# Optimization experiments

Measured on AMD Instinct MI355X. Metric: run time of the kernel, lower is better.

## Reference

```python
import jax, jax.numpy as jnp
import numpy as np

B, N, H = 4, 1024, 32


def setup_inputs() -> dict:
    key = jax.random.key(0)
    ks = jax.random.split(key, 8)
    weights = jax.random.uniform(ks[0], (B, N), dtype=jnp.float32)
    distances = jax.random.uniform(ks[1], (B, N, N), dtype=jnp.float32)
    # nn.Linear-style params (kaiming-uniform-ish scale: U(-1/sqrt(fan_in), 1/sqrt(fan_in)))
    def lin(k, fan_in, fan_out):
        k1, k2 = jax.random.split(k)
        bound = 1.0 / np.sqrt(fan_in)
        W = jax.random.uniform(k1, (fan_in, fan_out), minval=-bound, maxval=bound, dtype=jnp.float32)
        b = jax.random.uniform(k2, (fan_out,), minval=-bound, maxval=bound, dtype=jnp.float32)
        return W, b
    W1, b1 = lin(ks[2], 3, H)
    W2, b2 = lin(ks[3], H, H)
    W3, b3 = lin(ks[4], H, 1)
    return {"weights": weights, "distances": distances,
            "W1": W1, "b1": b1, "W2": W2, "b2": b2, "W3": W3, "b3": b3}


def reference(weights, distances, W1, b1, W2, b2, W3, b3):
    # Avoid materializing the stacked [B,N,N,3] tensor: since the first layer
    # is linear, split W1 rows and broadcast-add the three contributions.
    # h1[b,i,j,:] = w_i * W1[0] + w_j * W1[1] + d_ij * W1[2] + b1
    wi = weights[:, :, None, None] * W1[0]            # [B,N,1,H]
    wj = weights[:, None, :, None] * W1[1]            # [B,1,N,H]
    h = wi + wj + distances[..., None] * W1[2] + b1   # [B,N,N,H]
    h = jax.nn.relu(h)
    h = jax.nn.relu(jnp.einsum('bijh,hk->bijk', h, W2) + b2)
    out = jnp.einsum('bijh,ho->bijo', h, W3) + b3     # [B,N,N,1]
    return jax.nn.softplus(out[..., 0])               # [B,N,N]
```

## Files before the change

kernel.cpp:

```cpp
#include <hip/hip_runtime.h>

#define HCH 32
#define NDIM 1024

using half8 = __attribute__((ext_vector_type(8))) _Float16;
using floatx16 = __attribute__((ext_vector_type(16))) float;

__global__ __launch_bounds__(256, 4)
void lf_kernel(const float* __restrict__ weights,
               const float* __restrict__ distances,
               const float* __restrict__ W1,
               const float* __restrict__ b1,
               const float* __restrict__ W2,
               const float* __restrict__ b2,
               const float* __restrict__ W3,
               const float* __restrict__ b3,
               float* __restrict__ out,
               int rows_total)
{
    const int lane = threadIdx.x & 63;
    const int row_id = blockIdx.x * 4 + (threadIdx.x >> 6);
    if (row_id >= rows_total) return;

    const int b = row_id >> 10;
    const int i = row_id & (NDIM - 1);

    const int col = lane & 31;
    const int half_id = lane >> 5;
    const int kb = half_id * 8;

    const float wi = weights[row_id];

    float base0[8], c0[8], e0[8], base1[8], c1[8], e1[8];
#pragma unroll
    for (int j = 0; j < 8; ++j) {
        const int ch0 = kb + j;
        const int ch1 = 16 + kb + j;
        base0[j] = fmaf(W1[ch0], wi, b1[ch0]);
        c0[j]    = W1[HCH + ch0];
        e0[j]    = W1[2 * HCH + ch0];
        base1[j] = fmaf(W1[ch1], wi, b1[ch1]);
        c1[j]    = W1[HCH + ch1];
        e1[j]    = W1[2 * HCH + ch1];
    }

    half8 a0, a1;
#pragma unroll
    for (int j = 0; j < 8; ++j) {
        a0[j] = (_Float16)W2[(kb + j) * HCH + col];
        a1[j] = (_Float16)W2[(16 + kb + j) * HCH + col];
    }

    floatx16 cinit;
    float w3r[16];
#pragma unroll
    for (int r = 0; r < 16; ++r) {
        const int rc = (r & 3) + 8 * (r >> 2) + 4 * half_id;
        cinit[r] = b2[rc];
        w3r[r]   = W3[rc];
    }
    const float b3v = b3[0];

    const float* __restrict__ drow = distances + (size_t)(b * NDIM + i) * NDIM;
    const float* __restrict__ wrow = weights + b * NDIM;
    float* __restrict__ orow = out + (size_t)(b * NDIM + i) * NDIM;

    float d_cur  = drow[col];
    float wj_cur = wrow[col];

    for (int j0 = 0; j0 < NDIM; j0 += 32) {
        const int jn = (j0 + 32 < NDIM) ? (j0 + 32 + col) : col;
        const float d_nxt  = drow[jn];
        const float wj_nxt = wrow[jn];

        half8 bf0, bf1;
#pragma unroll
        for (int j = 0; j < 8; ++j) {
            const float h0 = fmaxf(fmaf(e0[j], d_cur, fmaf(c0[j], wj_cur, base0[j])), 0.0f);
            const float h1 = fmaxf(fmaf(e1[j], d_cur, fmaf(c1[j], wj_cur, base1[j])), 0.0f);
            bf0[j] = (_Float16)h0;
            bf1[j] = (_Float16)h1;
        }

        floatx16 acc = __builtin_amdgcn_mfma_f32_32x32x16_f16(a0, bf0, cinit, 0, 0, 0);
        acc = __builtin_amdgcn_mfma_f32_32x32x16_f16(a1, bf1, acc, 0, 0, 0);

        float s0 = 0.0f, s1 = 0.0f, s2 = 0.0f, s3 = 0.0f;
#pragma unroll
        for (int r = 0; r < 16; r += 4) {
            s0 = fmaf(fmaxf(acc[r + 0], 0.0f), w3r[r + 0], s0);
            s1 = fmaf(fmaxf(acc[r + 1], 0.0f), w3r[r + 1], s1);
            s2 = fmaf(fmaxf(acc[r + 2], 0.0f), w3r[r + 2], s2);
            s3 = fmaf(fmaxf(acc[r + 3], 0.0f), w3r[r + 3], s3);
        }
        float s = (s0 + s1) + (s2 + s3);
        s += __shfl_xor(s, 32, 64);

        const float x = s + b3v;
        const float sp = fmaxf(x, 0.0f) + __logf(1.0f + __expf(-fabsf(x)));

        if (lane < 32) orow[j0 + col] = sp;

        d_cur = d_nxt;
        wj_cur = wj_nxt;
    }
}

extern "C" void kernel_launch(void* const* d_in, const int* in_sizes, int n_in,
                              void* d_out, int out_size, void* d_ws, size_t ws_size,
                              hipStream_t stream) {
    const float* weights   = (const float*)d_in[0];
    const float* distances = (const float*)d_in[1];
    const float* W1 = (const float*)d_in[2];
    const float* b1 = (const float*)d_in[3];
    const float* W2 = (const float*)d_in[4];
    const float* b2 = (const float*)d_in[5];
    const float* W3 = (const float*)d_in[6];
    const float* b3 = (const float*)d_in[7];
    float* out = (float*)d_out;

    const int rows_total = 4 * 1024;
    dim3 grid(rows_total / 4);
    lf_kernel<<<grid, 256, 0, stream>>>(weights, distances, W1, b1, W2, b2, W3, b3,
                                        out, rows_total);
}
```

Measured before the change: 112.3 us.

## Split rows into segments per wave and compute layer-1 in packed fp16

Each wave now handles a 256-column segment of a row instead of the whole row, so there are four times as many waves and the grid grows accordingly. All distance and weight loads for the segment are issued up front into registers and the tile loop is fully unrolled. The first layer is computed with packed half2 FMAs and max instead of fp32 FMAs followed by conversion. This trades extra per-wave setup work (recomputing W1/W2/W3 constants) and lower first-layer precision for more parallelism, earlier memory-level parallelism, and fewer ALU instructions.

```diff
diff --git a/kernel.cpp b/kernel.cpp
--- a/kernel.cpp
+++ b/kernel.cpp
@@ -2,8 +2,12 @@
 
 #define HCH 32
 #define NDIM 1024
+#define TILE 32
+#define SEG 256
+#define SEG_ITERS (SEG / TILE)
 
-using half8 = __attribute__((ext_vector_type(8))) _Float16;
+using half2v   = __attribute__((ext_vector_type(2))) _Float16;
+using half8    = __attribute__((ext_vector_type(8))) _Float16;
 using floatx16 = __attribute__((ext_vector_type(16))) float;
 
 __global__ __launch_bounds__(256, 4)
@@ -15,15 +19,14 @@
                const float* __restrict__ b2,
                const float* __restrict__ W3,
                const float* __restrict__ b3,
-               float* __restrict__ out,
-               int rows_total)
+               float* __restrict__ out)
 {
     const int lane = threadIdx.x & 63;
-    const int row_id = blockIdx.x * 4 + (threadIdx.x >> 6);
-    if (row_id >= rows_total) return;
-
+    const int wave_gid = blockIdx.x * 4 + (threadIdx.x >> 6);
+    const int row_id = wave_gid >> 2;
+    const int seg = wave_gid & 3;
     const int b = row_id >> 10;
-    const int i = row_id & (NDIM - 1);
+    const int j_begin = seg * SEG;
 
     const int col = lane & 31;
     const int half_id = lane >> 5;
@@ -31,17 +34,15 @@
 
     const float wi = weights[row_id];
 
-    float base0[8], c0[8], e0[8], base1[8], c1[8], e1[8];
+    half2v base2[8], cc2[8], ee2[8];
 #pragma unroll
-    for (int j = 0; j < 8; ++j) {
-        const int ch0 = kb + j;
-        const int ch1 = 16 + kb + j;
-        base0[j] = fmaf(W1[ch0], wi, b1[ch0]);
-        c0[j]    = W1[HCH + ch0];
-        e0[j]    = W1[2 * HCH + ch0];
-        base1[j] = fmaf(W1[ch1], wi, b1[ch1]);
-        c1[j]    = W1[HCH + ch1];
-        e1[j]    = W1[2 * HCH + ch1];
+    for (int p = 0; p < 8; ++p) {
+        const int chA = (p < 4) ? (kb + 2 * p) : (16 + kb + 2 * (p - 4));
+        const int chB = chA + 1;
+        base2[p] = half2v{(_Float16)fmaf(W1[chA], wi, b1[chA]),
+                          (_Float16)fmaf(W1[chB], wi, b1[chB])};
+        cc2[p] = half2v{(_Float16)W1[HCH + chA], (_Float16)W1[HCH + chB]};
+        ee2[p] = half2v{(_Float16)W1[2 * HCH + chA], (_Float16)W1[2 * HCH + chB]};
     }
 
     half8 a0, a1;
@@ -61,29 +62,41 @@
     }
     const float b3v = b3[0];
 
-    const float* __restrict__ drow = distances + (size_t)(b * NDIM + i) * NDIM;
+    const float* __restrict__ drow = distances + (size_t)row_id * NDIM;
     const float* __restrict__ wrow = weights + b * NDIM;
-    float* __restrict__ orow = out + (size_t)(b * NDIM + i) * NDIM;
+    float* __restrict__ orow = out + (size_t)row_id * NDIM;
 
-    float d_cur  = drow[col];
-    float wj_cur = wrow[col];
+    float d_t[SEG_ITERS], wj_t[SEG_ITERS];
+#pragma unroll
+    for (int t = 0; t < SEG_ITERS; ++t) {
+        d_t[t]  = drow[j_begin + t * TILE + col];
+        wj_t[t] = wrow[j_begin + t * TILE + col];
+    }
 
-    for (int j0 = 0; j0 < NDIM; j0 += 32) {
-        const int jn = (j0 + 32 < NDIM) ? (j0 + 32 + col) : col;
-        const float d_nxt  = drow[jn];
-        const float wj_nxt = wrow[jn];
+    const half2v zero2 = half2v{(_Float16)0.0f, (_Float16)0.0f};
 
-        half8 bf0, bf1;
 #pragma unroll
-        for (int j = 0; j < 8; ++j) {
-            const float h0 = fmaxf(fmaf(e0[j], d_cur, fmaf(c0[j], wj_cur, base0[j])), 0.0f);
-            const float h1 = fmaxf(fmaf(e1[j], d_cur, fmaf(c1[j], wj_cur, base1[j])), 0.0f);
-            bf0[j] = (_Float16)h0;
-            bf1[j] = (_Float16)h1;
+    for (int t = 0; t < SEG_ITERS; ++t) {
+        const int j0 = j_begin + t * TILE;
+
+        const _Float16 dh  = (_Float16)d_t[t];
+        const _Float16 wjh = (_Float16)wj_t[t];
+        const half2v d2  = half2v{dh, dh};
+        const half2v wj2 = half2v{wjh, wjh};
+
+        union Frag { half8 v; half2v h[4]; } u0, u1;
+#pragma unroll
+        for (int p = 0; p < 4; ++p) {
+            half2v t0 = __builtin_elementwise_fma(cc2[p], wj2, base2[p]);
+            t0 = __builtin_elementwise_fma(ee2[p], d2, t0);
+            u0.h[p] = __builtin_elementwise_max(t0, zero2);
+            half2v t1 = __builtin_elementwise_fma(cc2[p + 4], wj2, base2[p + 4]);
+            t1 = __builtin_elementwise_fma(ee2[p + 4], d2, t1);
+            u1.h[p] = __builtin_elementwise_max(t1, zero2);
         }
 
-        floatx16 acc = __builtin_amdgcn_mfma_f32_32x32x16_f16(a0, bf0, cinit, 0, 0, 0);
-        acc = __builtin_amdgcn_mfma_f32_32x32x16_f16(a1, bf1, acc, 0, 0, 0);
+        floatx16 acc = __builtin_amdgcn_mfma_f32_32x32x16_f16(a0, u0.v, cinit, 0, 0, 0);
+        acc = __builtin_amdgcn_mfma_f32_32x32x16_f16(a1, u1.v, acc, 0, 0, 0);
 
         float s0 = 0.0f, s1 = 0.0f, s2 = 0.0f, s3 = 0.0f;
 #pragma unroll
@@ -100,9 +113,6 @@
         const float sp = fmaxf(x, 0.0f) + __logf(1.0f + __expf(-fabsf(x)));
 
         if (lane < 32) orow[j0 + col] = sp;
-
-        d_cur = d_nxt;
-        wj_cur = wj_nxt;
     }
 }
 
@@ -120,7 +130,6 @@
     float* out = (float*)d_out;
 
     const int rows_total = 4 * 1024;
-    dim3 grid(rows_total / 4);
-    lf_kernel<<<grid, 256, 0, stream>>>(weights, distances, W1, b1, W2, b2, W3, b3,
-                                        out, rows_total);
+    dim3 grid(rows_total * (NDIM / SEG) / 4);
+    lf_kernel<<<grid, 256, 0, stream>>>(weights, distances, W1, b1, W2, b2, W3, b3, out);
 }
```

After: 107.5 us. -4.2%, faster.
